# Performance work log

Measured on AMD Instinct MI355X. Metric: run time of the kernel, lower is better.

Reference implementation:

```python
import jax, jax.numpy as jnp
import numpy as np

N = 50000        # nodes
E = 800000       # edges (avg degree 16)
D = 128          # input_dim
H = 128          # hidden_channels
OUT = 1          # output_dim
NUM_GRAPHS = 512 # graphs in batch (fixed for jit; == batch.max()+1)


def setup_inputs() -> dict:
    key = jax.random.key(0)
    ks = jax.random.split(key, 12)
    x = jax.random.normal(ks[0], (N, D), dtype=jnp.float32)
    edge_index = jax.random.randint(ks[1], (2, E), 0, N, dtype=jnp.int64)
    batch = jnp.sort(jax.random.randint(ks[2], (N,), 0, NUM_GRAPHS, dtype=jnp.int64))
    init = lambda k, shape, fan: jax.random.normal(k, shape, jnp.float32) * np.float32(1.0 / np.sqrt(fan))
    W1 = init(ks[3], (D, H), D); b1 = jnp.zeros((H,), jnp.float32)
    W2 = init(ks[4], (H, H), H); b2 = jnp.zeros((H,), jnp.float32)
    W3 = init(ks[5], (H, H), H); b3 = jnp.zeros((H,), jnp.float32)
    Wo = init(ks[6], (H, OUT), H); bo = jnp.zeros((OUT,), jnp.float32)
    return {"x": x, "edge_index": edge_index, "batch": batch,
            "W1": W1, "b1": b1, "W2": W2, "b2": b2, "W3": W3, "b3": b3,
            "Wo": Wo, "bo": bo}


def _gcn_layer(h, W, b, src, dst, dinv_sqrt):
    # GCNConv: x' = D^{-1/2}(A+I)D^{-1/2} X W + b  (self-loops added)
    hw = h @ W                                        # [N, H]
    coef = (dinv_sqrt[src] * dinv_sqrt[dst])[:, None] # [E, 1]
    agg = jax.ops.segment_sum(hw[src] * coef, dst, num_segments=N)
    agg = agg + hw * (dinv_sqrt * dinv_sqrt)[:, None] # self-loop term: deg^{-1}
    return agg + b


def reference(x, edge_index, batch, W1, b1, W2, b2, W3, b3, Wo, bo):
    src, dst = edge_index[0], edge_index[1]
    # degree from A+I (PyG computes deg on the target/col index)
    deg = jax.ops.segment_sum(jnp.ones((E,), x.dtype), dst, num_segments=N) + 1.0
    dinv_sqrt = jax.lax.rsqrt(deg)
    h = jax.nn.relu(_gcn_layer(x, W1, b1, src, dst, dinv_sqrt))
    h = jax.nn.relu(_gcn_layer(h, W2, b2, src, dst, dinv_sqrt))
    h = _gcn_layer(h, W3, b3, src, dst, dinv_sqrt)   # last conv: no relu
    pooled = jax.ops.segment_sum(h, batch, num_segments=NUM_GRAPHS)  # global_add_pool
    # F.dropout(p=0.1) is identity in eval mode
    return pooled @ Wo + bo                           # [NUM_GRAPHS, 1]
```

## Files before the change

### kernel.cpp

```cpp
#include <hip/hip_runtime.h>

typedef _Float16 f16;
typedef unsigned short u16;
typedef __attribute__((ext_vector_type(2))) _Float16 f16x2;
typedef __attribute__((ext_vector_type(8))) _Float16 f16x8;
typedef __attribute__((ext_vector_type(8))) unsigned short u16x8;
typedef __attribute__((ext_vector_type(4))) float f32x4;
typedef __attribute__((ext_vector_type(4))) int intx4;

#define STRIDE 64

__device__ inline float2 h2f(unsigned u){
    f16x2 h = __builtin_bit_cast(f16x2, u);
    return make_float2((float)h.x, (float)h.y);
}

__device__ inline void addrow(float* acc, uint4 u){
    float2 p0 = h2f(u.x), p1 = h2f(u.y), p2 = h2f(u.z), p3 = h2f(u.w);
    acc[0] += p0.x; acc[1] += p0.y; acc[2] += p1.x; acc[3] += p1.y;
    acc[4] += p2.x; acc[5] += p2.y; acc[6] += p3.x; acc[7] += p3.y;
}


__global__ __launch_bounds__(256) void k_fillP(const int* __restrict__ src, const int* __restrict__ dst,
                                               int* __restrict__ fil, u16* __restrict__ csr, int E4, int E){
    int part  = blockIdx.x & 7;
    int chunk = blockIdx.x >> 3;
    int i4 = chunk*256 + threadIdx.x;
    if (i4 >= E4) return;
    intx4 d4 = __builtin_nontemporal_load((const intx4*)dst + i4);
    intx4 s4 = __builtin_nontemporal_load((const intx4*)src + i4);
    int base = i4*4;
    #pragma unroll
    for (int j = 0; j < 4; ++j){
        int e = base + j;
        int d = (j==0)?d4.x:(j==1)?d4.y:(j==2)?d4.z:d4.w;
        int s = (j==0)?s4.x:(j==1)?s4.y:(j==2)?s4.z:s4.w;
        if (e < E && (d & 7) == part){
            int p = atomicAdd(&fil[d], 1);
            if (p < STRIDE) csr[(size_t)d*STRIDE + p] = (u16)s;
        }
    }
}

__global__ __launch_bounds__(256) void k_finhist(const int* __restrict__ fil, float* __restrict__ dinv,
                                                 u16* __restrict__ csr, uint4* __restrict__ hwrows,
                                                 int* __restrict__ blkh, int N){
    __shared__ int h[8];
    int t = threadIdx.x;
    if (t < 8) h[t] = 0;
    __syncthreads();
    int i = blockIdx.x*256 + t;
    if (i < N){
        int cfull = fil[i];
        dinv[i] = rsqrtf((float)cfull + 1.0f);
        int cc = min(cfull, STRIDE);
        int pc = min((cc + 7) & ~7, STRIDE);
        for (int q = cc; q < pc; ++q) csr[(size_t)i*STRIDE + q] = (u16)N;
        int nb = (cc + 7) >> 3;
        if (nb > 7) nb = 7;
        atomicAdd(&h[nb], 1);
    }
    if (blockIdx.x == 0){
        if (t < 16) hwrows[(size_t)N*16 + t] = make_uint4(0,0,0,0);
        if (t == 16) dinv[N] = 0.f;
    }
    __syncthreads();
    if (t < 8) blkh[blockIdx.x*8 + t] = h[t];
}

__global__ __launch_bounds__(256) void k_bscan(const int* __restrict__ blkh, int* __restrict__ blkoff,
                                               int* __restrict__ ord, int N, int NQ4, int nbB){
    __shared__ int sm[8][256];
    int t = threadIdx.x;
    int v[8];
    #pragma unroll
    for (int b = 0; b < 8; ++b){
        v[b] = (t < nbB) ? blkh[t*8 + b] : 0;
        sm[b][t] = v[b];
    }
    __syncthreads();
    for (int off = 1; off < 256; off <<= 1){
        int u[8];
        #pragma unroll
        for (int b = 0; b < 8; ++b) u[b] = (t >= off) ? sm[b][t-off] : 0;
        __syncthreads();
        #pragma unroll
        for (int b = 0; b < 8; ++b) sm[b][t] += u[b];
        __syncthreads();
    }
    int s = 0;
    int bases[8];
    #pragma unroll
    for (int b = 0; b < 8; ++b){ bases[b] = s; s += sm[b][255]; }
    if (t < nbB){
        #pragma unroll
        for (int b = 0; b < 8; ++b)
            blkoff[t*8 + b] = sm[b][t] - v[b] + bases[b];
    }
    for (int i = N + t; i < NQ4; i += 256) ord[i] = N;
}

__global__ __launch_bounds__(256) void k_scatterL(const int* __restrict__ fil, const int* __restrict__ blkoff,
                                                  int* __restrict__ ord, int N){
    __shared__ int off[8];
    int t = threadIdx.x;
    if (t < 8) off[t] = blkoff[blockIdx.x*8 + t];
    __syncthreads();
    int i = blockIdx.x*256 + t;
    if (i < N){
        int nb = (min(fil[i], STRIDE) + 7) >> 3;
        if (nb > 7) nb = 7;
        int p = atomicAdd(&off[nb], 1);
        ord[p] = i;
    }
}


__global__ __launch_bounds__(128) void k_prep(const float* __restrict__ W3, const float* __restrict__ Wo,
                                              const float* __restrict__ b3, float* __restrict__ u,
                                              float* __restrict__ su, float* __restrict__ zs, int N){
    __shared__ float sWo[128];
    __shared__ float red[128];
    int t = threadIdx.x;
    sWo[t] = Wo[t];
    __syncthreads();
    float s = 0.f;
    for (int c2 = 0; c2 < 128; ++c2) s = fmaf(W3[t*128 + c2], sWo[c2], s);
    u[t] = s;
    red[t] = b3[t] * sWo[t];
    __syncthreads();
    for (int o = 64; o > 0; o >>= 1){
        if (t < o) red[t] += red[t+o];
        __syncthreads();
    }
    if (t == 0){ *su = red[0]; zs[N] = 0.f; }
}


#define LDW 136

template<int AFP16>
__global__ __launch_bounds__(256) void k_mm(const void* __restrict__ Av, const float* __restrict__ W,
                                            const float* __restrict__ dinv, f16* __restrict__ C, int n){
    __shared__ __align__(16) _Float16 sWt[128*LDW];
    __shared__ __align__(16) _Float16 sOut[4][16*LDW];
    int t = threadIdx.x;
    for (int idx = t; idx < 4096; idx += 256){
        int k = idx >> 5, c4 = (idx & 31) * 4;
        float4 w = ((const float4*)W)[idx];
        sWt[(c4+0)*LDW + k] = (f16)w.x;
        sWt[(c4+1)*LDW + k] = (f16)w.y;
        sWt[(c4+2)*LDW + k] = (f16)w.z;
        sWt[(c4+3)*LDW + k] = (f16)w.w;
    }
    __syncthreads();

    int wv = t >> 6, l = t & 63;
    int r16 = l & 15, g = l >> 4;
    int r0 = blockIdx.x * 64 + wv * 16;

    int arow = r0 + r16;
    bool aok = arow < n;
    f16x8 a[4];
    #pragma unroll
    for (int s = 0; s < 4; ++s){
        if (AFP16){
            const f16* A = (const f16*)Av;
            a[s] = aok ? *(const f16x8*)&A[(size_t)arow*128 + s*32 + g*8] : (f16x8)(_Float16)0.f;
        } else {
            const float* A = (const float*)Av;
            f16x8 av = (f16x8)(_Float16)0.f;
            if (aok){
                const float4* ap = (const float4*)&A[(size_t)arow*128 + s*32 + g*8];
                float4 x0 = ap[0], x1 = ap[1];
                av[0]=(f16)x0.x; av[1]=(f16)x0.y; av[2]=(f16)x0.z; av[3]=(f16)x0.w;
                av[4]=(f16)x1.x; av[5]=(f16)x1.y; av[6]=(f16)x1.z; av[7]=(f16)x1.w;
            }
            a[s] = av;
        }
    }

    f32x4 acc[8];
    #pragma unroll
    for (int ct = 0; ct < 8; ++ct) acc[ct] = (f32x4)0.f;

    #pragma unroll
    for (int ct = 0; ct < 8; ++ct){
        int c = ct*16 + r16;
        #pragma unroll
        for (int s = 0; s < 4; ++s){
            f16x8 b = *(const f16x8*)&sWt[c*LDW + s*32 + g*8];
            acc[ct] = __builtin_amdgcn_mfma_f32_16x16x32_f16(a[s], b, acc[ct], 0, 0, 0);
        }
    }

    float dv[4];
    #pragma unroll
    for (int j = 0; j < 4; ++j){
        int rr = r0 + g*4 + j;
        dv[j] = (rr < n) ? dinv[rr] : 0.f;
    }
    #pragma unroll
    for (int ct = 0; ct < 8; ++ct)
        #pragma unroll
        for (int j = 0; j < 4; ++j)
            sOut[wv][(g*4+j)*LDW + ct*16 + r16] = (f16)(acc[ct][j] * dv[j]);
    __syncthreads();

    int orow = r0 + r16;
    if (orow < n){
        const f16x8* srcp = (const f16x8*)&sOut[wv][r16*LDW + g*32];
        f16x8 o0 = srcp[0], o1 = srcp[1], o2 = srcp[2], o3 = srcp[3];
        f16x8* dstp = (f16x8*)&C[(size_t)orow*128 + g*32];
        dstp[0]=o0; dstp[1]=o1; dstp[2]=o2; dstp[3]=o3;
    }
}


#define AGG_BODY \
    int l = threadIdx.x & 63; \
    int g = l >> 4, c = l & 15; \
    intx4 wq = *((const intx4*)ord + wvi); \
    int w0 = __builtin_amdgcn_readfirstlane(wq.x); \
    int w1 = __builtin_amdgcn_readfirstlane(wq.y); \
    int w2 = __builtin_amdgcn_readfirstlane(wq.z); \
    int w3 = __builtin_amdgcn_readfirstlane(wq.w); \
    int wsel = (g==0) ? w0 : (g==1) ? w1 : (g==2) ? w2 : w3; \
    const uint4* rows = (const uint4*)hw; \
    float acc[8] = {0,0,0,0,0,0,0,0}; \
    { uint4 s = rows[(size_t)wsel*16 + c]; addrow(acc, s); } \
    int nb0=(min(fil[w0],STRIDE)+7)>>3, nb1=(min(fil[w1],STRIDE)+7)>>3; \
    int nb2=(min(fil[w2],STRIDE)+7)>>3, nb3=(min(fil[w3],STRIDE)+7)>>3; \
    int nbm  = max(max(nb0,nb1), max(nb2,nb3)); \
    int nbsel = (g==0) ? nb0 : (g==1) ? nb1 : (g==2) ? nb2 : nb3; \
    const u16* cp = csr + (size_t)wsel*STRIDE; \
    for (int t2 = 0; t2 < nbm; ++t2){ \
        if (t2 < nbsel){ \
            u16x8 iv = *(const u16x8*)cp; cp += 8; \
            uint4 r0 = rows[(size_t)iv[0]*16 + c]; \
            uint4 r1 = rows[(size_t)iv[1]*16 + c]; \
            uint4 r2 = rows[(size_t)iv[2]*16 + c]; \
            uint4 r3 = rows[(size_t)iv[3]*16 + c]; \
            uint4 r4 = rows[(size_t)iv[4]*16 + c]; \
            uint4 r5 = rows[(size_t)iv[5]*16 + c]; \
            uint4 r6 = rows[(size_t)iv[6]*16 + c]; \
            uint4 r7 = rows[(size_t)iv[7]*16 + c]; \
            addrow(acc, r0); addrow(acc, r1); addrow(acc, r2); addrow(acc, r3); \
            addrow(acc, r4); addrow(acc, r5); addrow(acc, r6); addrow(acc, r7); \
        } \
    }

__global__ __launch_bounds__(256) void k_agg4(const f16* __restrict__ hw, const float* __restrict__ dinv,
                                              const int* __restrict__ fil, const u16* __restrict__ csr,
                                              const int* __restrict__ ord, const float* __restrict__ bias,
                                              f16* __restrict__ hout, int N, int NQ){
    int wvi = (blockIdx.x*256 + threadIdx.x) >> 6;
    if (wvi >= NQ) return;
    AGG_BODY
    if (wsel < N){
        float di = dinv[wsel];
        const float4* bp = (const float4*)bias + c*2;
        float4 b0 = bp[0], b1 = bp[1];
        f16x8 o;
        o[0]=(f16)fmaxf(fmaf(acc[0],di,b0.x),0.f); o[1]=(f16)fmaxf(fmaf(acc[1],di,b0.y),0.f);
        o[2]=(f16)fmaxf(fmaf(acc[2],di,b0.z),0.f); o[3]=(f16)fmaxf(fmaf(acc[3],di,b0.w),0.f);
        o[4]=(f16)fmaxf(fmaf(acc[4],di,b1.x),0.f); o[5]=(f16)fmaxf(fmaf(acc[5],di,b1.y),0.f);
        o[6]=(f16)fmaxf(fmaf(acc[6],di,b1.z),0.f); o[7]=(f16)fmaxf(fmaf(acc[7],di,b1.w),0.f);
        *(f16x8*)&hout[(size_t)wsel*128 + c*8] = o;
    }
}

__global__ __launch_bounds__(256) void k_agg4z(const f16* __restrict__ hw, const float* __restrict__ dinv,
                                               const int* __restrict__ fil, const u16* __restrict__ csr,
                                               const int* __restrict__ ord, const float* __restrict__ bias,
                                               const float* __restrict__ u, float* __restrict__ zs,
                                               int N, int NQ){
    int wvi = (blockIdx.x*256 + threadIdx.x) >> 6;
    if (wvi >= NQ) return;
    AGG_BODY
    float di = dinv[wsel];
    const float4* bp = (const float4*)bias + c*2;
    const float4* up = (const float4*)u    + c*2;
    float4 b0 = bp[0], b1 = bp[1];
    float4 u0 = up[0], u1 = up[1];
    float dot = fmaxf(fmaf(acc[0],di,b0.x),0.f)*u0.x + fmaxf(fmaf(acc[1],di,b0.y),0.f)*u0.y
              + fmaxf(fmaf(acc[2],di,b0.z),0.f)*u0.z + fmaxf(fmaf(acc[3],di,b0.w),0.f)*u0.w
              + fmaxf(fmaf(acc[4],di,b1.x),0.f)*u1.x + fmaxf(fmaf(acc[5],di,b1.y),0.f)*u1.y
              + fmaxf(fmaf(acc[6],di,b1.z),0.f)*u1.z + fmaxf(fmaf(acc[7],di,b1.w),0.f)*u1.w;
    dot += __shfl_xor(dot, 1);
    dot += __shfl_xor(dot, 2);
    dot += __shfl_xor(dot, 4);
    dot += __shfl_xor(dot, 8);
    if (c == 0 && wsel < N) zs[wsel] = di * dot;
}


__global__ __launch_bounds__(256) void k_aggs(const float* __restrict__ zs, const float* __restrict__ dinv,
                                              const int* __restrict__ fil, const u16* __restrict__ csr,
                                              const int* __restrict__ batch, const float* __restrict__ supt,
                                              float* __restrict__ out, int N){
    __shared__ float bins[512];
    int t = threadIdx.x;
    bins[t] = 0.f; bins[t+256] = 0.f;
    __syncthreads();
    int i = blockIdx.x*256 + t;
    if (i < N){
        float acc = zs[i];
        int nb = (min(fil[i], STRIDE) + 7) >> 3;
        const u16* cp = csr + (size_t)i*STRIDE;
        for (int b = 0; b < nb; ++b){
            u16x8 iv = *(const u16x8*)cp; cp += 8;
            float s0 = zs[iv[0]] + zs[iv[1]], s1 = zs[iv[2]] + zs[iv[3]];
            float s2 = zs[iv[4]] + zs[iv[5]], s3 = zs[iv[6]] + zs[iv[7]];
            acc += (s0 + s1) + (s2 + s3);
        }
        float tv = fmaf(dinv[i], acc, *supt);
        atomicAdd(&bins[batch[i]], tv);
    }
    __syncthreads();
    float v0 = bins[t], v1 = bins[t+256];
    if (v0 != 0.f) atomicAdd(&out[t], v0);
    if (v1 != 0.f) atomicAdd(&out[t+256], v1);
}

__global__ __launch_bounds__(256) void k_init_out(float* __restrict__ out, const float* __restrict__ bo, int G){
    int g = blockIdx.x*256 + threadIdx.x;
    if (g < G) out[g] = bo[0];
}


extern "C" void kernel_launch(void* const* d_in, const int* in_sizes, int n_in,
                              void* d_out, int out_size, void* d_ws, size_t ws_size,
                              hipStream_t stream) {
    const float* x     = (const float*)d_in[0];
    const int*   ei    = (const int*)d_in[1];
    const int*   batch = (const int*)d_in[2];
    const float* W1 = (const float*)d_in[3];
    const float* b1 = (const float*)d_in[4];
    const float* W2 = (const float*)d_in[5];
    const float* b2 = (const float*)d_in[6];
    const float* W3 = (const float*)d_in[7];
    const float* b3 = (const float*)d_in[8];
    const float* Wo = (const float*)d_in[9];
    const float* bo = (const float*)d_in[10];

    int N = in_sizes[0] / 128;
    int E = in_sizes[1] / 2;
    int G = out_size;
    const int* srcI = ei;
    const int* dstI = ei + E;

    int NQ  = (N + 3) / 4;
    int NQ4 = NQ * 4;
    int nbN = (N + 255)/256;
    int E4  = (E + 3)/4;
    int nbF = 8 * ((E4 + 255)/256);

    char* p = (char*)d_ws;
    size_t off = 0;
    auto alloc = [&](size_t bytes) -> void* {
        void* r = p + off;
        off += (bytes + 255) & ~(size_t)255;
        return r;
    };
    f16*   hw     = (f16*)alloc((size_t)(N+1)*128*sizeof(f16));
    f16*   h      = (f16*)alloc((size_t)N*128*sizeof(f16));
    float* dinv   = (float*)alloc((size_t)(N+1)*sizeof(float));
    int*   fil    = (int*)alloc((size_t)(N+1)*sizeof(int));
    int*   blkh   = (int*)alloc((size_t)nbN*8*sizeof(int));
    int*   blkoff = (int*)alloc((size_t)nbN*8*sizeof(int));
    int*   ord    = (int*)alloc((size_t)NQ4*sizeof(int));
    float* zs     = (float*)alloc((size_t)(N+1)*sizeof(float));
    float* uvec   = (float*)alloc(128*sizeof(float));
    float* su     = (float*)alloc(sizeof(float));
    u16*   csr    = (u16*)alloc((size_t)(N+1)*STRIDE*sizeof(u16));

    hipMemsetAsync(fil, 0, (size_t)(N+1)*sizeof(int), stream);

    k_fillP   <<<nbF, 256, 0, stream>>>(srcI, dstI, fil, csr, E4, E);
    k_finhist <<<nbN, 256, 0, stream>>>(fil, dinv, csr, (uint4*)hw, blkh, N);
    k_bscan   <<<1,   256, 0, stream>>>(blkh, blkoff, ord, N, NQ4, nbN);
    k_scatterL<<<nbN, 256, 0, stream>>>(fil, blkoff, ord, N);
    k_prep    <<<1,   128, 0, stream>>>(W3, Wo, b3, uvec, su, zs, N);

    int nbM = (N + 63)/64;
    int nbA = (int)(((size_t)NQ*64 + 255)/256);

    k_mm<0> <<<nbM, 256, 0, stream>>>(x, W1, dinv, hw, N);
    k_agg4  <<<nbA, 256, 0, stream>>>(hw, dinv, fil, csr, ord, b1, h, N, NQ);
    k_mm<1> <<<nbM, 256, 0, stream>>>(h, W2, dinv, hw, N);
    k_agg4z <<<nbA, 256, 0, stream>>>(hw, dinv, fil, csr, ord, b2, uvec, zs, N, NQ);
    k_init_out<<<(G + 255)/256, 256, 0, stream>>>((float*)d_out, bo, G);
    k_aggs  <<<nbN, 256, 0, stream>>>(zs, dinv, fil, csr, batch, su, (float*)d_out, N);
}
```

Measured before the change: 183.9 us.

## Build CSR via two-pass bucketed counting sort in shared memory

Replaces the global-atomic CSR fill, which was partitioned by node parity, with a two-stage scheme. First, edges are bucketed by dst>>8 into fixed-size slabs using block-local histograms. Then each block builds 256 node rows in shared memory (XOR-swizzled) and writes them out coalesced, along with counts, dinv and histogram. Output init and zero-row setup are folded into existing kernels to drop a launch. This adds an intermediate buffer write/read and silently drops edges if a bucket exceeds SLAB.

```diff
diff --git a/kernel.cpp b/kernel.cpp
--- a/kernel.cpp
+++ b/kernel.cpp
@@ -9,6 +9,7 @@
 typedef __attribute__((ext_vector_type(4))) int intx4;
 
 #define STRIDE 64
+#define SLAB   5120
 
 __device__ inline float2 h2f(unsigned u){
     f16x2 h = __builtin_bit_cast(f16x2, u);
@@ -22,55 +23,90 @@
 }
 
 
-__global__ __launch_bounds__(256) void k_fillP(const int* __restrict__ src, const int* __restrict__ dst,
-                                               int* __restrict__ fil, u16* __restrict__ csr, int E4, int E){
-    int part  = blockIdx.x & 7;
-    int chunk = blockIdx.x >> 3;
-    int i4 = chunk*256 + threadIdx.x;
-    if (i4 >= E4) return;
-    intx4 d4 = __builtin_nontemporal_load((const intx4*)dst + i4);
-    intx4 s4 = __builtin_nontemporal_load((const intx4*)src + i4);
-    int base = i4*4;
-    #pragma unroll
-    for (int j = 0; j < 4; ++j){
-        int e = base + j;
-        int d = (j==0)?d4.x:(j==1)?d4.y:(j==2)?d4.z:d4.w;
-        int s = (j==0)?s4.x:(j==1)?s4.y:(j==2)?s4.z:s4.w;
-        if (e < E && (d & 7) == part){
-            int p = atomicAdd(&fil[d], 1);
-            if (p < STRIDE) csr[(size_t)d*STRIDE + p] = (u16)s;
-        }
-    }
-}
-
-__global__ __launch_bounds__(256) void k_finhist(const int* __restrict__ fil, float* __restrict__ dinv,
-                                                 u16* __restrict__ csr, uint4* __restrict__ hwrows,
-                                                 int* __restrict__ blkh, int N){
-    __shared__ int h[8];
-    int t = threadIdx.x;
-    if (t < 8) h[t] = 0;
-    __syncthreads();
-    int i = blockIdx.x*256 + t;
-    if (i < N){
-        int cfull = fil[i];
-        dinv[i] = rsqrtf((float)cfull + 1.0f);
-        int cc = min(cfull, STRIDE);
-        int pc = min((cc + 7) & ~7, STRIDE);
-        for (int q = cc; q < pc; ++q) csr[(size_t)i*STRIDE + q] = (u16)N;
-        int nb = (cc + 7) >> 3;
-        if (nb > 7) nb = 7;
-        atomicAdd(&h[nb], 1);
-    }
-    if (blockIdx.x == 0){
-        if (t < 16) hwrows[(size_t)N*16 + t] = make_uint4(0,0,0,0);
-        if (t == 16) dinv[N] = 0.f;
-    }
-    __syncthreads();
-    if (t < 8) blkh[blockIdx.x*8 + t] = h[t];
+__global__ __launch_bounds__(256) void k_bucket(const int* __restrict__ src, const int* __restrict__ dst,
+                                                int* __restrict__ bucketCnt, unsigned* __restrict__ bucketBuf,
+                                                int NB, int E4, int E){
+    __shared__ int hist[256], pos[256];
+    int t = threadIdx.x;
+    hist[t] = 0;
+    __syncthreads();
+    int i4a = blockIdx.x*512 + t;
+    int i4b = i4a + 256;
+    bool va = i4a < E4, vb = i4b < E4;
+    intx4 da = {}, db = {}, sa = {}, sb = {};
+    if (va){ da = __builtin_nontemporal_load((const intx4*)dst + i4a);
+             sa = __builtin_nontemporal_load((const intx4*)src + i4a); }
+    if (vb){ db = __builtin_nontemporal_load((const intx4*)dst + i4b);
+             sb = __builtin_nontemporal_load((const intx4*)src + i4b); }
+    auto cnt1 = [&](int e, int d){ if (e < E) atomicAdd(&hist[d >> 8], 1); };
+    if (va){ int b0 = i4a*4; cnt1(b0,da.x); cnt1(b0+1,da.y); cnt1(b0+2,da.z); cnt1(b0+3,da.w); }
+    if (vb){ int b0 = i4b*4; cnt1(b0,db.x); cnt1(b0+1,db.y); cnt1(b0+2,db.z); cnt1(b0+3,db.w); }
+    __syncthreads();
+    if (t < NB && hist[t] > 0) pos[t] = atomicAdd(&bucketCnt[t], hist[t]);
+    __syncthreads();
+    auto put1 = [&](int e, int d, int s){
+        if (e < E){
+            int b = d >> 8;
+            int slot = atomicAdd(&pos[b], 1);
+            if (slot < SLAB)
+                bucketBuf[(size_t)b*SLAB + slot] = ((unsigned)(d & 255) << 16) | (unsigned)s;
+        }
+    };
+    if (va){ int b0 = i4a*4; put1(b0,da.x,sa.x); put1(b0+1,da.y,sa.y); put1(b0+2,da.z,sa.z); put1(b0+3,da.w,sa.w); }
+    if (vb){ int b0 = i4b*4; put1(b0,db.x,sb.x); put1(b0+1,db.y,sb.y); put1(b0+2,db.z,sb.z); put1(b0+3,db.w,sb.w); }
+}
+
+
+__global__ __launch_bounds__(256) void k_build(const unsigned* __restrict__ bucketBuf,
+                                               const int* __restrict__ bucketCnt,
+                                               u16* __restrict__ csr, int* __restrict__ fil,
+                                               float* __restrict__ dinv, int* __restrict__ blkh, int N){
+    __shared__ u16 rows[256*64];
+    __shared__ int cnt[256];
+    __shared__ int h8[8];
+    int t = threadIdx.x;
+    cnt[t] = 0;
+    if (t < 8) h8[t] = 0;
+    u16x8 fillv;
+    #pragma unroll
+    for (int j = 0; j < 8; ++j) fillv[j] = (u16)N;
+    #pragma unroll
+    for (int j = 0; j < 8; ++j) *(u16x8*)&rows[t*64 + j*8] = fillv;
+    __syncthreads();
+    int b = blockIdx.x;
+    int cb = min(bucketCnt[b], SLAB);
+    for (int e = t; e < cb; e += 256){
+        unsigned v = bucketBuf[(size_t)b*SLAB + e];
+        int off = v >> 16;
+        int p = atomicAdd(&cnt[off], 1);
+        if (p < STRIDE){
+            int ch = ((p >> 3) ^ (off & 7));
+            rows[off*64 + ch*8 + (p & 7)] = (u16)(v & 0xffff);
+        }
+    }
+    __syncthreads();
+    int node = b*256 + t;
+    if (node <= N){
+        int c = cnt[t];
+        fil[node] = c;
+        dinv[node] = rsqrtf((float)c + 1.0f);
+        if (node < N){
+            int nb = (min(c, STRIDE) + 7) >> 3;
+            if (nb > 7) nb = 7;
+            atomicAdd(&h8[nb], 1);
+        }
+        u16x8* d8 = (u16x8*)&csr[(size_t)node*64];
+        #pragma unroll
+        for (int j = 0; j < 8; ++j)
+            d8[j] = *(u16x8*)&rows[t*64 + ((j ^ (t & 7))*8)];
+    }
+    __syncthreads();
+    if (t < 8) blkh[b*8 + t] = h8[t];
 }
 
 __global__ __launch_bounds__(256) void k_bscan(const int* __restrict__ blkh, int* __restrict__ blkoff,
-                                               int* __restrict__ ord, int N, int NQ4, int nbB){
+                                               int* __restrict__ ord, uint4* __restrict__ hwrows,
+                                               int N, int NQ4, int nbB){
     __shared__ int sm[8][256];
     int t = threadIdx.x;
     int v[8];
@@ -98,6 +134,7 @@
         for (int b = 0; b < 8; ++b)
             blkoff[t*8 + b] = sm[b][t] - v[b] + bases[b];
     }
+    if (t >= 200 && t < 216) hwrows[(size_t)N*16 + (t - 200)] = make_uint4(0,0,0,0);
     for (int i = N + t; i < NQ4; i += 256) ord[i] = N;
 }
 
@@ -119,7 +156,9 @@
 
 __global__ __launch_bounds__(128) void k_prep(const float* __restrict__ W3, const float* __restrict__ Wo,
                                               const float* __restrict__ b3, float* __restrict__ u,
-                                              float* __restrict__ su, float* __restrict__ zs, int N){
+                                              float* __restrict__ su, float* __restrict__ zs,
+                                              float* __restrict__ out, const float* __restrict__ bo,
+                                              int N, int G){
     __shared__ float sWo[128];
     __shared__ float red[128];
     int t = threadIdx.x;
@@ -135,6 +174,8 @@
         __syncthreads();
     }
     if (t == 0){ *su = red[0]; zs[N] = 0.f; }
+    float bv = bo[0];
+    for (int g2 = t; g2 < G; g2 += 128) out[g2] = bv;
 }
 
 
@@ -324,11 +365,6 @@
     if (v1 != 0.f) atomicAdd(&out[t+256], v1);
 }
 
-__global__ __launch_bounds__(256) void k_init_out(float* __restrict__ out, const float* __restrict__ bo, int G){
-    int g = blockIdx.x*256 + threadIdx.x;
-    if (g < G) out[g] = bo[0];
-}
-
 
 extern "C" void kernel_launch(void* const* d_in, const int* in_sizes, int n_in,
                               void* d_out, int out_size, void* d_ws, size_t ws_size,
@@ -353,9 +389,9 @@
 
     int NQ  = (N + 3) / 4;
     int NQ4 = NQ * 4;
-    int nbN = (N + 255)/256;
-    int E4  = (E + 3)/4;
-    int nbF = 8 * ((E4 + 255)/256);
+    int NB  = (N + 256) / 256;
+    int E4  = (E + 3) / 4;
+    int nbK = (E + 2047) / 2048;
 
     char* p = (char*)d_ws;
     size_t off = 0;
@@ -364,25 +400,27 @@
         off += (bytes + 255) & ~(size_t)255;
         return r;
     };
-    f16*   hw     = (f16*)alloc((size_t)(N+1)*128*sizeof(f16));
-    f16*   h      = (f16*)alloc((size_t)N*128*sizeof(f16));
-    float* dinv   = (float*)alloc((size_t)(N+1)*sizeof(float));
-    int*   fil    = (int*)alloc((size_t)(N+1)*sizeof(int));
-    int*   blkh   = (int*)alloc((size_t)nbN*8*sizeof(int));
-    int*   blkoff = (int*)alloc((size_t)nbN*8*sizeof(int));
-    int*   ord    = (int*)alloc((size_t)NQ4*sizeof(int));
-    float* zs     = (float*)alloc((size_t)(N+1)*sizeof(float));
-    float* uvec   = (float*)alloc(128*sizeof(float));
-    float* su     = (float*)alloc(sizeof(float));
-    u16*   csr    = (u16*)alloc((size_t)(N+1)*STRIDE*sizeof(u16));
-
-    hipMemsetAsync(fil, 0, (size_t)(N+1)*sizeof(int), stream);
-
-    k_fillP   <<<nbF, 256, 0, stream>>>(srcI, dstI, fil, csr, E4, E);
-    k_finhist <<<nbN, 256, 0, stream>>>(fil, dinv, csr, (uint4*)hw, blkh, N);
-    k_bscan   <<<1,   256, 0, stream>>>(blkh, blkoff, ord, N, NQ4, nbN);
-    k_scatterL<<<nbN, 256, 0, stream>>>(fil, blkoff, ord, N);
-    k_prep    <<<1,   128, 0, stream>>>(W3, Wo, b3, uvec, su, zs, N);
+    f16*      hw      = (f16*)alloc((size_t)(N+1)*128*sizeof(f16));
+    f16*      h       = (f16*)alloc((size_t)N*128*sizeof(f16));
+    float*    dinv    = (float*)alloc((size_t)(N+1)*sizeof(float));
+    int*      fil     = (int*)alloc((size_t)(N+1)*sizeof(int));
+    int*      blkh    = (int*)alloc((size_t)NB*8*sizeof(int));
+    int*      blkoff  = (int*)alloc((size_t)NB*8*sizeof(int));
+    int*      ord     = (int*)alloc((size_t)NQ4*sizeof(int));
+    float*    zs      = (float*)alloc((size_t)(N+1)*sizeof(float));
+    float*    uvec    = (float*)alloc(128*sizeof(float));
+    float*    su      = (float*)alloc(sizeof(float));
+    int*      bucketCnt = (int*)alloc((size_t)NB*sizeof(int));
+    unsigned* bucketBuf = (unsigned*)alloc((size_t)NB*SLAB*sizeof(unsigned));
+    u16*      csr     = (u16*)alloc((size_t)(N+1)*STRIDE*sizeof(u16));
+
+    hipMemsetAsync(bucketCnt, 0, (size_t)NB*sizeof(int), stream);
+
+    k_bucket  <<<nbK, 256, 0, stream>>>(srcI, dstI, bucketCnt, bucketBuf, NB, E4, E);
+    k_build   <<<NB,  256, 0, stream>>>(bucketBuf, bucketCnt, csr, fil, dinv, blkh, N);
+    k_bscan   <<<1,   256, 0, stream>>>(blkh, blkoff, ord, (uint4*)hw, N, NQ4, NB);
+    k_scatterL<<<NB,  256, 0, stream>>>(fil, blkoff, ord, N);
+    k_prep    <<<1,   128, 0, stream>>>(W3, Wo, b3, uvec, su, zs, (float*)d_out, bo, N, G);
 
     int nbM = (N + 63)/64;
     int nbA = (int)(((size_t)NQ*64 + 255)/256);
@@ -391,6 +429,5 @@
     k_agg4  <<<nbA, 256, 0, stream>>>(hw, dinv, fil, csr, ord, b1, h, N, NQ);
     k_mm<1> <<<nbM, 256, 0, stream>>>(h, W2, dinv, hw, N);
     k_agg4z <<<nbA, 256, 0, stream>>>(hw, dinv, fil, csr, ord, b2, uvec, zs, N, NQ);
-    k_init_out<<<(G + 255)/256, 256, 0, stream>>>((float*)d_out, bo, G);
-    k_aggs  <<<nbN, 256, 0, stream>>>(zs, dinv, fil, csr, batch, su, (float*)d_out, N);
-}
+    k_aggs  <<<NB,  256, 0, stream>>>(zs, dinv, fil, csr, batch, su, (float*)d_out, N);
+}
```

Result: faster. 161.6 us (-12.1%).
